# Kernel tuning notes

Measured on AMD Instinct MI355X. Metric: run time of the kernel, lower is better.

Reference implementation:

```python
import jax, jax.numpy as jnp
import numpy as np

N_NODES = 200000
D_FEAT = 128
B = 40000
DEG = 16
E = B * DEG
D_OUT = 256
N_CLASSES = 128


def setup_inputs() -> dict:
    key = jax.random.key(0)
    ks = jax.random.split(key, 8)
    inputs = jax.random.randint(ks[0], (B,), 0, N_NODES)
    neighbor_ids = jax.random.randint(ks[1], (E,), 0, N_NODES)
    segment_ids = jnp.repeat(jnp.arange(B, dtype=jnp.int64 if jax.config.jax_enable_x64 else jnp.int32), DEG)
    feat_data = jax.random.normal(ks[2], (N_NODES, D_FEAT), dtype=jnp.float32)
    W1 = jax.random.normal(ks[3], (D_OUT, 2 * D_FEAT), dtype=jnp.float32) * 0.05
    b1 = jax.random.normal(ks[4], (D_OUT,), dtype=jnp.float32) * 0.05
    W3 = jax.random.normal(ks[5], (N_CLASSES, D_OUT), dtype=jnp.float32) * 0.05
    b3 = jax.random.normal(ks[6], (N_CLASSES,), dtype=jnp.float32) * 0.05
    return {"inputs": inputs, "neighbor_ids": neighbor_ids, "segment_ids": segment_ids,
            "feat_data": feat_data, "W1": W1, "b1": b1, "W3": W3, "b3": b3}


def reference(inputs, neighbor_ids, segment_ids, feat_data, W1, b1, W3, b3):
    # Segment-mean over neighbor features (replaces Python per-node loop)
    neigh = feat_data[neighbor_ids]                               # [E, D]
    sums = jax.ops.segment_sum(neigh, segment_ids, num_segments=B)  # [B, D]
    cnt = jax.ops.segment_sum(jnp.ones((E,), jnp.float32), segment_ids, num_segments=B)
    means = sums / jnp.maximum(cnt, 1.0)[:, None]                 # [B, D]
    # Concat self + neighbor-mean, linear1
    emb = jnp.concatenate([feat_data[inputs], means], axis=1)     # [B, 2D]
    h = emb @ W1.T + b1                                           # [B, D_OUT]
    # ReLU -> linear3 -> L2 normalize (F.normalize, eps=1e-12)
    logits = jax.nn.relu(h) @ W3.T + b3                           # [B, n_classes]
    norm = jnp.linalg.norm(logits, axis=1, keepdims=True)
    return logits / jnp.maximum(norm, 1e-12)
```

## Files before the change

### kernel.cpp

```cpp
#include <hip/hip_runtime.h>
#include <stdint.h>

#define NNODES 200000
#define BNODES 40000
#define DEG    16
#define DFEAT  128
#define DOUT   256
#define NCLS   128
#define TILE   32

typedef __attribute__((ext_vector_type(8))) __bf16 bf16x8;
typedef __attribute__((ext_vector_type(4))) float  floatx4;

__device__ __forceinline__ uint32_t f2bf(float f) {
  uint32_t x = __float_as_uint(f);
  return ((x + 0x7fffu + ((x >> 16) & 1u)) >> 16) & 0xffffu;
}

__global__ void cvt_weights(const float* __restrict__ W1, const float* __restrict__ W3,
                            uint16_t* __restrict__ w1b, uint16_t* __restrict__ w3b) {
  int i = blockIdx.x * 256 + threadIdx.x;
  if (i < DOUT * 2 * DFEAT) w1b[i] = (uint16_t)f2bf(W1[i]);
  if (i < NCLS * DOUT)      w3b[i] = (uint16_t)f2bf(W3[i]);
}

__global__ __launch_bounds__(256) void sage_fused(
    const int* __restrict__ inputs, const int* __restrict__ nbr,
    const float* __restrict__ feat,
    const uint16_t* __restrict__ w1b, const float* __restrict__ b1,
    const uint16_t* __restrict__ w3b, const float* __restrict__ b3,
    float* __restrict__ out) {
  __shared__ __align__(16) uint16_t embL[TILE][264];
  __shared__ __align__(16) uint16_t hL[TILE][264];
  __shared__ __align__(16) float    lgL[TILE][132];

  const int tid  = threadIdx.x;
  const int w    = tid >> 6;
  const int lane = tid & 63;
  const int quad = lane >> 4;
  const int l16  = lane & 15;

  {
    const int nodeBase = blockIdx.x * TILE + w * 8;
#pragma unroll
    for (int n = 0; n < 8; ++n) {
      const int node = nodeBase + n;
      const int row  = w * 8 + n;
      const int* nb  = nbr + node * DEG;
      float sx = 0.f, sy = 0.f;
#pragma unroll
      for (int j = 0; j < DEG; ++j) {
        const float2 v = *(const float2*)(feat + (size_t)nb[j] * DFEAT + lane * 2);
        sx += v.x; sy += v.y;
      }
      const float2 sv = *(const float2*)(feat + (size_t)inputs[node] * DFEAT + lane * 2);
      const uint32_t selfp = f2bf(sv.x) | (f2bf(sv.y) << 16);
      const uint32_t meanp = f2bf(sx * 0.0625f) | (f2bf(sy * 0.0625f) << 16);
      *(uint32_t*)&embL[row][lane * 2]         = selfp;
      *(uint32_t*)&embL[row][DFEAT + lane * 2] = meanp;
    }
  }
  __syncthreads();

  const int kq = quad * 8;

  {
    floatx4 acc[2][4];
#pragma unroll
    for (int mt = 0; mt < 2; ++mt)
#pragma unroll
      for (int ot = 0; ot < 4; ++ot) {
        floatx4 z = {0.f, 0.f, 0.f, 0.f};
        acc[mt][ot] = z;
      }
#pragma unroll
    for (int kt = 0; kt < 8; ++kt) {
      const int k0 = kt * 32 + kq;
      const bf16x8 a0 = *(const bf16x8*)&embL[l16][k0];
      const bf16x8 a1 = *(const bf16x8*)&embL[16 + l16][k0];
#pragma unroll
      for (int ot = 0; ot < 4; ++ot) {
        const int o = (w * 4 + ot) * 16 + l16;
        const bf16x8 b = *(const bf16x8*)(w1b + o * 256 + k0);
        acc[0][ot] = __builtin_amdgcn_mfma_f32_16x16x32_bf16(a0, b, acc[0][ot], 0, 0, 0);
        acc[1][ot] = __builtin_amdgcn_mfma_f32_16x16x32_bf16(a1, b, acc[1][ot], 0, 0, 0);
      }
    }
#pragma unroll
    for (int ot = 0; ot < 4; ++ot) {
      const int o = (w * 4 + ot) * 16 + l16;
      const float bias = b1[o];
#pragma unroll
      for (int mt = 0; mt < 2; ++mt)
#pragma unroll
        for (int r = 0; r < 4; ++r) {
          float v = acc[mt][ot][r] + bias;
          v = fmaxf(v, 0.f);
          hL[mt * 16 + quad * 4 + r][o] = (uint16_t)f2bf(v);
        }
    }
  }
  __syncthreads();

  {
    floatx4 acc2[2][2];
#pragma unroll
    for (int mt = 0; mt < 2; ++mt)
#pragma unroll
      for (int ct = 0; ct < 2; ++ct) {
        floatx4 z = {0.f, 0.f, 0.f, 0.f};
        acc2[mt][ct] = z;
      }
#pragma unroll
    for (int kt = 0; kt < 8; ++kt) {
      const int k0 = kt * 32 + kq;
      const bf16x8 a0 = *(const bf16x8*)&hL[l16][k0];
      const bf16x8 a1 = *(const bf16x8*)&hL[16 + l16][k0];
#pragma unroll
      for (int ct = 0; ct < 2; ++ct) {
        const int c = (w * 2 + ct) * 16 + l16;
        const bf16x8 b = *(const bf16x8*)(w3b + c * 256 + k0);
        acc2[0][ct] = __builtin_amdgcn_mfma_f32_16x16x32_bf16(a0, b, acc2[0][ct], 0, 0, 0);
        acc2[1][ct] = __builtin_amdgcn_mfma_f32_16x16x32_bf16(a1, b, acc2[1][ct], 0, 0, 0);
      }
    }
#pragma unroll
    for (int ct = 0; ct < 2; ++ct) {
      const int c = (w * 2 + ct) * 16 + l16;
      const float bias = b3[c];
#pragma unroll
      for (int mt = 0; mt < 2; ++mt)
#pragma unroll
        for (int r = 0; r < 4; ++r)
          lgL[mt * 16 + quad * 4 + r][c] = acc2[mt][ct][r] + bias;
    }
  }
  __syncthreads();

  {
    const int nr  = tid >> 3;
    const int sub = tid & 7;
    const float* lrow = &lgL[nr][sub * 16];
    float4 v0 = *(const float4*)(lrow + 0);
    float4 v1 = *(const float4*)(lrow + 4);
    float4 v2 = *(const float4*)(lrow + 8);
    float4 v3 = *(const float4*)(lrow + 12);
    float ss = v0.x * v0.x + v0.y * v0.y + v0.z * v0.z + v0.w * v0.w
             + v1.x * v1.x + v1.y * v1.y + v1.z * v1.z + v1.w * v1.w
             + v2.x * v2.x + v2.y * v2.y + v2.z * v2.z + v2.w * v2.w
             + v3.x * v3.x + v3.y * v3.y + v3.z * v3.z + v3.w * v3.w;
    ss += __shfl_xor(ss, 1);
    ss += __shfl_xor(ss, 2);
    ss += __shfl_xor(ss, 4);
    const float scale = 1.f / fmaxf(sqrtf(ss), 1e-12f);
    v0.x *= scale; v0.y *= scale; v0.z *= scale; v0.w *= scale;
    v1.x *= scale; v1.y *= scale; v1.z *= scale; v1.w *= scale;
    v2.x *= scale; v2.y *= scale; v2.z *= scale; v2.w *= scale;
    v3.x *= scale; v3.y *= scale; v3.z *= scale; v3.w *= scale;
    float* op = out + ((size_t)(blockIdx.x * TILE + nr)) * NCLS + sub * 16;
    *(float4*)(op + 0)  = v0;
    *(float4*)(op + 4)  = v1;
    *(float4*)(op + 8)  = v2;
    *(float4*)(op + 12) = v3;
  }
}

extern "C" void kernel_launch(void* const* d_in, const int* in_sizes, int n_in,
                              void* d_out, int out_size, void* d_ws, size_t ws_size,
                              hipStream_t stream) {
  const int*   inputs = (const int*)d_in[0];
  const int*   nbr    = (const int*)d_in[1];
  const float* feat   = (const float*)d_in[3];
  const float* W1     = (const float*)d_in[4];
  const float* b1     = (const float*)d_in[5];
  const float* W3     = (const float*)d_in[6];
  const float* b3     = (const float*)d_in[7];

  uint16_t* w1b = (uint16_t*)d_ws;
  uint16_t* w3b = w1b + DOUT * 2 * DFEAT;

  cvt_weights<<<(DOUT * 2 * DFEAT) / 256, 256, 0, stream>>>(W1, W3, w1b, w3b);
  sage_fused<<<BNODES / TILE, 256, 0, stream>>>(inputs, nbr, feat, w1b, b1, w3b, b3,
                                                (float*)d_out);
}
```

Measured before the change: 218.0 us.

## Vectorize neighbor gather with float4 loads and overlap all row fetches

The gather stage now has each half-wave process one node, using 16-byte loads per lane. All 16 neighbor indices are fetched as int4 vectors and all 17 feature rows are loaded before summing, to raise memory-level parallelism on the random gather. The embedding and logits LDS buffers are aliased to cut shared memory, and launch bounds request 4 blocks per CU to raise occupancy. This costs more live registers per thread.

```diff
diff --git a/kernel.cpp b/kernel.cpp
--- a/kernel.cpp
+++ b/kernel.cpp
@@ -24,15 +24,16 @@
   if (i < NCLS * DOUT)      w3b[i] = (uint16_t)f2bf(W3[i]);
 }
 
-__global__ __launch_bounds__(256) void sage_fused(
+__global__ __launch_bounds__(256, 4) void sage_fused(
     const int* __restrict__ inputs, const int* __restrict__ nbr,
     const float* __restrict__ feat,
     const uint16_t* __restrict__ w1b, const float* __restrict__ b1,
     const uint16_t* __restrict__ w3b, const float* __restrict__ b3,
     float* __restrict__ out) {
-  __shared__ __align__(16) uint16_t embL[TILE][264];
+  __shared__ __align__(16) unsigned char smemA[TILE * 264 * 2];
   __shared__ __align__(16) uint16_t hL[TILE][264];
-  __shared__ __align__(16) float    lgL[TILE][132];
+  uint16_t (*embL)[264] = (uint16_t (*)[264])smemA;
+  float    (*lgL)[132]  = (float    (*)[132])smemA;
 
   const int tid  = threadIdx.x;
   const int w    = tid >> 6;
@@ -41,23 +42,38 @@
   const int l16  = lane & 15;
 
   {
+    const int h   = lane >> 5;
+    const int l32 = lane & 31;
+    const int col = l32 * 4;
     const int nodeBase = blockIdx.x * TILE + w * 8;
-#pragma unroll
-    for (int n = 0; n < 8; ++n) {
-      const int node = nodeBase + n;
-      const int row  = w * 8 + n;
+    const float* fb = feat + col;
+#pragma unroll
+    for (int p = 0; p < 4; ++p) {
+      const int node = nodeBase + p * 2 + h;
+      const int row  = w * 8 + p * 2 + h;
       const int* nb  = nbr + node * DEG;
-      float sx = 0.f, sy = 0.f;
-#pragma unroll
-      for (int j = 0; j < DEG; ++j) {
-        const float2 v = *(const float2*)(feat + (size_t)nb[j] * DFEAT + lane * 2);
-        sx += v.x; sy += v.y;
-      }
-      const float2 sv = *(const float2*)(feat + (size_t)inputs[node] * DFEAT + lane * 2);
-      const uint32_t selfp = f2bf(sv.x) | (f2bf(sv.y) << 16);
-      const uint32_t meanp = f2bf(sx * 0.0625f) | (f2bf(sy * 0.0625f) << 16);
-      *(uint32_t*)&embL[row][lane * 2]         = selfp;
-      *(uint32_t*)&embL[row][DFEAT + lane * 2] = meanp;
+      const int4 i0 = *(const int4*)(nb + 0);
+      const int4 i1 = *(const int4*)(nb + 4);
+      const int4 i2 = *(const int4*)(nb + 8);
+      const int4 i3 = *(const int4*)(nb + 12);
+      const int self = inputs[node];
+#define LDN(name, idx) const floatx4 name = *(const floatx4*)(fb + (size_t)(idx) * DFEAT)
+      LDN(v0,  i0.x); LDN(v1,  i0.y); LDN(v2,  i0.z); LDN(v3,  i0.w);
+      LDN(v4,  i1.x); LDN(v5,  i1.y); LDN(v6,  i1.z); LDN(v7,  i1.w);
+      LDN(v8,  i2.x); LDN(v9,  i2.y); LDN(v10, i2.z); LDN(v11, i2.w);
+      LDN(v12, i3.x); LDN(v13, i3.y); LDN(v14, i3.z); LDN(v15, i3.w);
+      LDN(sv, self);
+#undef LDN
+      const floatx4 s = (((v0 + v1) + (v2 + v3)) + ((v4 + v5) + (v6 + v7)))
+                      + (((v8 + v9) + (v10 + v11)) + ((v12 + v13) + (v14 + v15)));
+      const floatx4 m = s * 0.0625f;
+      uint2 selfp, meanp;
+      selfp.x = f2bf(sv.x) | (f2bf(sv.y) << 16);
+      selfp.y = f2bf(sv.z) | (f2bf(sv.w) << 16);
+      meanp.x = f2bf(m.x) | (f2bf(m.y) << 16);
+      meanp.y = f2bf(m.z) | (f2bf(m.w) << 16);
+      *(uint2*)&embL[row][col]         = selfp;
+      *(uint2*)&embL[row][DFEAT + col] = meanp;
     }
   }
   __syncthreads();
```

Measured after the change: 212.8 us. 2.3% less time.

## Widen neighbor gathers to 16-byte loads split across half-wavefronts, alias LDS buffers

Applied to the files above, without the earlier changes.

The gather phase now has each half-wavefront read a different neighbor row with float4 loads and combines the halves with a cross-lane shuffle. Two nodes are processed per iteration, so 16 independent loads are in flight per lane. The LDS buffers for the embedding tile and the logits tile now share storage, and launch bounds request 4 blocks per CU to raise occupancy. The cost is more registers per thread and extra shuffle work, which could limit how many waves fit on a CU.

```diff
diff --git a/kernel.cpp b/kernel.cpp
--- a/kernel.cpp
+++ b/kernel.cpp
@@ -17,47 +17,90 @@
   return ((x + 0x7fffu + ((x >> 16) & 1u)) >> 16) & 0xffffu;
 }
 
-__global__ void cvt_weights(const float* __restrict__ W1, const float* __restrict__ W3,
-                            uint16_t* __restrict__ w1b, uint16_t* __restrict__ w3b) {
+__global__ __launch_bounds__(256) void cvt_weights(
+    const float* __restrict__ W1, const float* __restrict__ W3,
+    uint16_t* __restrict__ w1b, uint16_t* __restrict__ w3b) {
   int i = blockIdx.x * 256 + threadIdx.x;
   if (i < DOUT * 2 * DFEAT) w1b[i] = (uint16_t)f2bf(W1[i]);
   if (i < NCLS * DOUT)      w3b[i] = (uint16_t)f2bf(W3[i]);
 }
 
-__global__ __launch_bounds__(256) void sage_fused(
+__global__ __launch_bounds__(256, 4) void sage_fused(
     const int* __restrict__ inputs, const int* __restrict__ nbr,
     const float* __restrict__ feat,
     const uint16_t* __restrict__ w1b, const float* __restrict__ b1,
     const uint16_t* __restrict__ w3b, const float* __restrict__ b3,
     float* __restrict__ out) {
-  __shared__ __align__(16) uint16_t embL[TILE][264];
+  __shared__ __align__(16) unsigned char smemA[TILE * 264 * 2];
   __shared__ __align__(16) uint16_t hL[TILE][264];
-  __shared__ __align__(16) float    lgL[TILE][132];
+  uint16_t (*embL)[264] = (uint16_t (*)[264])smemA;
+  float    (*lgL)[132]  = (float    (*)[132])smemA;
 
   const int tid  = threadIdx.x;
-  const int w    = tid >> 6;
+  const int w    = __builtin_amdgcn_readfirstlane(tid >> 6);
   const int lane = tid & 63;
   const int quad = lane >> 4;
   const int l16  = lane & 15;
 
   {
+    const int h   = lane >> 5;
+    const int l32 = lane & 31;
     const int nodeBase = blockIdx.x * TILE + w * 8;
-#pragma unroll
-    for (int n = 0; n < 8; ++n) {
-      const int node = nodeBase + n;
-      const int row  = w * 8 + n;
-      const int* nb  = nbr + node * DEG;
-      float sx = 0.f, sy = 0.f;
-#pragma unroll
-      for (int j = 0; j < DEG; ++j) {
-        const float2 v = *(const float2*)(feat + (size_t)nb[j] * DFEAT + lane * 2);
-        sx += v.x; sy += v.y;
-      }
-      const float2 sv = *(const float2*)(feat + (size_t)inputs[node] * DFEAT + lane * 2);
-      const uint32_t selfp = f2bf(sv.x) | (f2bf(sv.y) << 16);
-      const uint32_t meanp = f2bf(sx * 0.0625f) | (f2bf(sy * 0.0625f) << 16);
-      *(uint32_t*)&embL[row][lane * 2]         = selfp;
-      *(uint32_t*)&embL[row][DFEAT + lane * 2] = meanp;
+    const float* fcol = feat + l32 * 4;
+#pragma unroll
+    for (int pp = 0; pp < 8; pp += 2) {
+      const int nodeA = nodeBase + pp;
+      const int nodeB = nodeBase + pp + 1;
+      const int* nbA = nbr + nodeA * DEG;
+      const int* nbB = nbr + nodeB * DEG;
+      const int selfA = inputs[nodeA];
+      const int selfB = inputs[nodeB];
+      floatx4 a0, a1, a2, a3, a4, a5, a6, a7;
+      floatx4 c0, c1, c2, c3, c4, c5, c6, c7;
+#define LDP(dst, nb, g)                                                      \
+  {                                                                          \
+    const int id_ = h ? (nb)[2 * (g) + 1] : (nb)[2 * (g)];                   \
+    dst = *(const floatx4*)(fcol + (size_t)id_ * DFEAT);                     \
+  }
+      LDP(a0, nbA, 0) LDP(a1, nbA, 1) LDP(a2, nbA, 2) LDP(a3, nbA, 3)
+      LDP(a4, nbA, 4) LDP(a5, nbA, 5) LDP(a6, nbA, 6) LDP(a7, nbA, 7)
+      const float2 svA = *(const float2*)(feat + (size_t)selfA * DFEAT + lane * 2);
+      LDP(c0, nbB, 0) LDP(c1, nbB, 1) LDP(c2, nbB, 2) LDP(c3, nbB, 3)
+      LDP(c4, nbB, 4) LDP(c5, nbB, 5) LDP(c6, nbB, 6) LDP(c7, nbB, 7)
+      const float2 svB = *(const float2*)(feat + (size_t)selfB * DFEAT + lane * 2);
+#undef LDP
+      {
+        floatx4 s = ((a0 + a1) + (a2 + a3)) + ((a4 + a5) + (a6 + a7));
+        s.x += __shfl_xor(s.x, 32);
+        s.y += __shfl_xor(s.y, 32);
+        s.z += __shfl_xor(s.z, 32);
+        s.w += __shfl_xor(s.w, 32);
+        const floatx4 m = s * 0.0625f;
+        const int row = w * 8 + pp;
+        *(uint32_t*)&embL[row][lane * 2] = f2bf(svA.x) | (f2bf(svA.y) << 16);
+        if (h == 0) {
+          uint2 mp;
+          mp.x = f2bf(m.x) | (f2bf(m.y) << 16);
+          mp.y = f2bf(m.z) | (f2bf(m.w) << 16);
+          *(uint2*)&embL[row][DFEAT + l32 * 4] = mp;
+        }
+      }
+      {
+        floatx4 s = ((c0 + c1) + (c2 + c3)) + ((c4 + c5) + (c6 + c7));
+        s.x += __shfl_xor(s.x, 32);
+        s.y += __shfl_xor(s.y, 32);
+        s.z += __shfl_xor(s.z, 32);
+        s.w += __shfl_xor(s.w, 32);
+        const floatx4 m = s * 0.0625f;
+        const int row = w * 8 + pp + 1;
+        *(uint32_t*)&embL[row][lane * 2] = f2bf(svB.x) | (f2bf(svB.y) << 16);
+        if (h == 0) {
+          uint2 mp;
+          mp.x = f2bf(m.x) | (f2bf(m.y) << 16);
+          mp.y = f2bf(m.z) | (f2bf(m.w) << 16);
+          *(uint2*)&embL[row][DFEAT + l32 * 4] = mp;
+        }
+      }
     }
   }
   __syncthreads();
```

Result: no change. 218.9 us (+0.4%).

## Pre-convert feature table to bf16 and gather bf16 rows with smaller tiles

Applied to the files above, without the earlier changes.

Adds a kernel that converts the whole feature table to bf16 in workspace each call, so the neighbor gather reads half the bytes per row. The tile is halved to 16 nodes with more blocks and higher occupancy, gathers are batched per node pair for more memory-level parallelism, and the embedding buffer is aliased with the logits buffer in shared memory. The cost is a full extra read and write pass over the 100MB feature table per call, and neighbor sums are now taken over rounded values. If the workspace is too small it falls back to an fp32 path.

```diff
diff --git a/kernel.cpp b/kernel.cpp
--- a/kernel.cpp
+++ b/kernel.cpp
@@ -7,7 +7,7 @@
 #define DFEAT  128
 #define DOUT   256
 #define NCLS   128
-#define TILE   32
+#define TILE   16
 
 typedef __attribute__((ext_vector_type(8))) __bf16 bf16x8;
 typedef __attribute__((ext_vector_type(4))) float  floatx4;
@@ -16,48 +16,122 @@
   uint32_t x = __float_as_uint(f);
   return ((x + 0x7fffu + ((x >> 16) & 1u)) >> 16) & 0xffffu;
 }
-
-__global__ void cvt_weights(const float* __restrict__ W1, const float* __restrict__ W3,
-                            uint16_t* __restrict__ w1b, uint16_t* __restrict__ w3b) {
+__device__ __forceinline__ float bf2f(uint16_t u) {
+  return __uint_as_float((uint32_t)u << 16);
+}
+
+__global__ __launch_bounds__(256) void cvt_weights(
+    const float* __restrict__ W1, const float* __restrict__ W3,
+    uint16_t* __restrict__ w1b, uint16_t* __restrict__ w3b) {
   int i = blockIdx.x * 256 + threadIdx.x;
   if (i < DOUT * 2 * DFEAT) w1b[i] = (uint16_t)f2bf(W1[i]);
   if (i < NCLS * DOUT)      w3b[i] = (uint16_t)f2bf(W3[i]);
 }
 
-__global__ __launch_bounds__(256) void sage_fused(
+__global__ __launch_bounds__(256) void cvt_feat(
+    const float* __restrict__ feat, uint16_t* __restrict__ featb) {
+  const size_t i = ((size_t)blockIdx.x * 256 + threadIdx.x) * 16;
+  const float4 f0 = *(const float4*)(feat + i + 0);
+  const float4 f1 = *(const float4*)(feat + i + 4);
+  const float4 f2 = *(const float4*)(feat + i + 8);
+  const float4 f3 = *(const float4*)(feat + i + 12);
+  uint4 p0, p1;
+  p0.x = f2bf(f0.x) | (f2bf(f0.y) << 16);
+  p0.y = f2bf(f0.z) | (f2bf(f0.w) << 16);
+  p0.z = f2bf(f1.x) | (f2bf(f1.y) << 16);
+  p0.w = f2bf(f1.z) | (f2bf(f1.w) << 16);
+  p1.x = f2bf(f2.x) | (f2bf(f2.y) << 16);
+  p1.y = f2bf(f2.z) | (f2bf(f2.w) << 16);
+  p1.z = f2bf(f3.x) | (f2bf(f3.y) << 16);
+  p1.w = f2bf(f3.z) | (f2bf(f3.w) << 16);
+  *(uint4*)(featb + i)     = p0;
+  *(uint4*)(featb + i + 8) = p1;
+}
+
+template <bool BF16T>
+__global__ __launch_bounds__(256, 8) void sage_fused(
     const int* __restrict__ inputs, const int* __restrict__ nbr,
-    const float* __restrict__ feat,
+    const float* __restrict__ feat, const uint16_t* __restrict__ featb,
     const uint16_t* __restrict__ w1b, const float* __restrict__ b1,
     const uint16_t* __restrict__ w3b, const float* __restrict__ b3,
     float* __restrict__ out) {
-  __shared__ __align__(16) uint16_t embL[TILE][264];
+  __shared__ __align__(16) unsigned char smemA[TILE * 264 * 2];
   __shared__ __align__(16) uint16_t hL[TILE][264];
-  __shared__ __align__(16) float    lgL[TILE][132];
+  uint16_t (*embL)[264] = (uint16_t (*)[264])smemA;
+  float    (*lgL)[132]  = (float    (*)[132])smemA;
 
   const int tid  = threadIdx.x;
-  const int w    = tid >> 6;
+  const int w    = __builtin_amdgcn_readfirstlane(tid >> 6);
   const int lane = tid & 63;
   const int quad = lane >> 4;
   const int l16  = lane & 15;
 
   {
-    const int nodeBase = blockIdx.x * TILE + w * 8;
-#pragma unroll
-    for (int n = 0; n < 8; ++n) {
-      const int node = nodeBase + n;
-      const int row  = w * 8 + n;
-      const int* nb  = nbr + node * DEG;
-      float sx = 0.f, sy = 0.f;
-#pragma unroll
-      for (int j = 0; j < DEG; ++j) {
-        const float2 v = *(const float2*)(feat + (size_t)nb[j] * DFEAT + lane * 2);
-        sx += v.x; sy += v.y;
-      }
-      const float2 sv = *(const float2*)(feat + (size_t)inputs[node] * DFEAT + lane * 2);
-      const uint32_t selfp = f2bf(sv.x) | (f2bf(sv.y) << 16);
-      const uint32_t meanp = f2bf(sx * 0.0625f) | (f2bf(sy * 0.0625f) << 16);
-      *(uint32_t*)&embL[row][lane * 2]         = selfp;
-      *(uint32_t*)&embL[row][DFEAT + lane * 2] = meanp;
+    const int nodeBase = blockIdx.x * TILE + w * 4;
+    if constexpr (BF16T) {
+      const uint16_t* fb = featb + lane * 2;
+#pragma unroll
+      for (int p = 0; p < 4; p += 2) {
+        const int nA = nodeBase + p, nB = nodeBase + p + 1;
+        const int* nbA = nbr + nA * DEG;
+        const int* nbB = nbr + nB * DEG;
+        const int sA = inputs[nA], sB = inputs[nB];
+        ushort2 rA[16], rB[16];
+#pragma unroll
+        for (int j = 0; j < 16; ++j)
+          rA[j] = *(const ushort2*)(fb + (size_t)nbA[j] * DFEAT);
+        const ushort2 svA = *(const ushort2*)(fb + (size_t)sA * DFEAT);
+#pragma unroll
+        for (int j = 0; j < 16; ++j)
+          rB[j] = *(const ushort2*)(fb + (size_t)nbB[j] * DFEAT);
+        const ushort2 svB = *(const ushort2*)(fb + (size_t)sB * DFEAT);
+        {
+          const float sx = (((bf2f(rA[0].x) + bf2f(rA[1].x)) + (bf2f(rA[2].x) + bf2f(rA[3].x)))
+                          + ((bf2f(rA[4].x) + bf2f(rA[5].x)) + (bf2f(rA[6].x) + bf2f(rA[7].x))))
+                         + (((bf2f(rA[8].x) + bf2f(rA[9].x)) + (bf2f(rA[10].x) + bf2f(rA[11].x)))
+                          + ((bf2f(rA[12].x) + bf2f(rA[13].x)) + (bf2f(rA[14].x) + bf2f(rA[15].x))));
+          const float sy = (((bf2f(rA[0].y) + bf2f(rA[1].y)) + (bf2f(rA[2].y) + bf2f(rA[3].y)))
+                          + ((bf2f(rA[4].y) + bf2f(rA[5].y)) + (bf2f(rA[6].y) + bf2f(rA[7].y))))
+                         + (((bf2f(rA[8].y) + bf2f(rA[9].y)) + (bf2f(rA[10].y) + bf2f(rA[11].y)))
+                          + ((bf2f(rA[12].y) + bf2f(rA[13].y)) + (bf2f(rA[14].y) + bf2f(rA[15].y))));
+          const int row = w * 4 + p;
+          *(uint32_t*)&embL[row][lane * 2]         = (uint32_t)svA.x | ((uint32_t)svA.y << 16);
+          *(uint32_t*)&embL[row][DFEAT + lane * 2] = f2bf(sx * 0.0625f) | (f2bf(sy * 0.0625f) << 16);
+        }
+        {
+          const float sx = (((bf2f(rB[0].x) + bf2f(rB[1].x)) + (bf2f(rB[2].x) + bf2f(rB[3].x)))
+                          + ((bf2f(rB[4].x) + bf2f(rB[5].x)) + (bf2f(rB[6].x) + bf2f(rB[7].x))))
+                         + (((bf2f(rB[8].x) + bf2f(rB[9].x)) + (bf2f(rB[10].x) + bf2f(rB[11].x)))
+                          + ((bf2f(rB[12].x) + bf2f(rB[13].x)) + (bf2f(rB[14].x) + bf2f(rB[15].x))));
+          const float sy = (((bf2f(rB[0].y) + bf2f(rB[1].y)) + (bf2f(rB[2].y) + bf2f(rB[3].y)))
+                          + ((bf2f(rB[4].y) + bf2f(rB[5].y)) + (bf2f(rB[6].y) + bf2f(rB[7].y))))
+                         + (((bf2f(rB[8].y) + bf2f(rB[9].y)) + (bf2f(rB[10].y) + bf2f(rB[11].y)))
+                          + ((bf2f(rB[12].y) + bf2f(rB[13].y)) + (bf2f(rB[14].y) + bf2f(rB[15].y))));
+          const int row = w * 4 + p + 1;
+          *(uint32_t*)&embL[row][lane * 2]         = (uint32_t)svB.x | ((uint32_t)svB.y << 16);
+          *(uint32_t*)&embL[row][DFEAT + lane * 2] = f2bf(sx * 0.0625f) | (f2bf(sy * 0.0625f) << 16);
+        }
+      }
+    } else {
+      const float* fb = feat + lane * 2;
+#pragma unroll
+      for (int p = 0; p < 4; ++p) {
+        const int node = nodeBase + p;
+        const int* nb  = nbr + node * DEG;
+        const int self = inputs[node];
+        float2 r[16];
+#pragma unroll
+        for (int j = 0; j < 16; ++j)
+          r[j] = *(const float2*)(fb + (size_t)nb[j] * DFEAT);
+        const float2 sv = *(const float2*)(fb + (size_t)self * DFEAT);
+        const float sx = (((r[0].x + r[1].x) + (r[2].x + r[3].x)) + ((r[4].x + r[5].x) + (r[6].x + r[7].x)))
+                       + (((r[8].x + r[9].x) + (r[10].x + r[11].x)) + ((r[12].x + r[13].x) + (r[14].x + r[15].x)));
+        const float sy = (((r[0].y + r[1].y) + (r[2].y + r[3].y)) + ((r[4].y + r[5].y) + (r[6].y + r[7].y)))
+                       + (((r[8].y + r[9].y) + (r[10].y + r[11].y)) + ((r[12].y + r[13].y) + (r[14].y + r[15].y)));
+        const int row = w * 4 + p;
+        *(uint32_t*)&embL[row][lane * 2]         = f2bf(sv.x) | (f2bf(sv.y) << 16);
+        *(uint32_t*)&embL[row][DFEAT + lane * 2] = f2bf(sx * 0.0625f) | (f2bf(sy * 0.0625f) << 16);
+      }
     }
   }
   __syncthreads();
@@ -65,103 +139,84 @@
   const int kq = quad * 8;
 
   {
-    floatx4 acc[2][4];
-#pragma unroll
-    for (int mt = 0; mt < 2; ++mt)
-#pragma unroll
-      for (int ot = 0; ot < 4; ++ot) {
-        floatx4 z = {0.f, 0.f, 0.f, 0.f};
-        acc[mt][ot] = z;
-      }
+    floatx4 acc[4];
+#pragma unroll
+    for (int ot = 0; ot < 4; ++ot) {
+      floatx4 z = {0.f, 0.f, 0.f, 0.f};
+      acc[ot] = z;
+    }
 #pragma unroll
     for (int kt = 0; kt < 8; ++kt) {
       const int k0 = kt * 32 + kq;
-      const bf16x8 a0 = *(const bf16x8*)&embL[l16][k0];
-      const bf16x8 a1 = *(const bf16x8*)&embL[16 + l16][k0];
+      const bf16x8 a = *(const bf16x8*)&embL[l16][k0];
 #pragma unroll
       for (int ot = 0; ot < 4; ++ot) {
-        const int o = (w * 4 + ot) * 16 + l16;
+        const int o = w * 64 + ot * 16 + l16;
         const bf16x8 b = *(const bf16x8*)(w1b + o * 256 + k0);
-        acc[0][ot] = __builtin_amdgcn_mfma_f32_16x16x32_bf16(a0, b, acc[0][ot], 0, 0, 0);
-        acc[1][ot] = __builtin_amdgcn_mfma_f32_16x16x32_bf16(a1, b, acc[1][ot], 0, 0, 0);
+        acc[ot] = __builtin_amdgcn_mfma_f32_16x16x32_bf16(a, b, acc[ot], 0, 0, 0);
       }
     }
 #pragma unroll
     for (int ot = 0; ot < 4; ++ot) {
-      const int o = (w * 4 + ot) * 16 + l16;
+      const int o = w * 64 + ot * 16 + l16;
       const float bias = b1[o];
 #pragma unroll
-      for (int mt = 0; mt < 2; ++mt)
-#pragma unroll
-        for (int r = 0; r < 4; ++r) {
-          float v = acc[mt][ot][r] + bias;
-          v = fmaxf(v, 0.f);
-          hL[mt * 16 + quad * 4 + r][o] = (uint16_t)f2bf(v);
-        }
+      for (int r = 0; r < 4; ++r) {
+        float v = acc[ot][r] + bias;
+        v = fmaxf(v, 0.f);
+        hL[quad * 4 + r][o] = (uint16_t)f2bf(v);
+      }
     }
   }
   __syncthreads();
 
   {
-    floatx4 acc2[2][2];
-#pragma unroll
-    for (int mt = 0; mt < 2; ++mt)
-#pragma unroll
-      for (int ct = 0; ct < 2; ++ct) {
-        floatx4 z = {0.f, 0.f, 0.f, 0.f};
-        acc2[mt][ct] = z;
-      }
+    floatx4 acc2[2];
+#pragma unroll
+    for (int ct = 0; ct < 2; ++ct) {
+      floatx4 z = {0.f, 0.f, 0.f, 0.f};
+      acc2[ct] = z;
+    }
 #pragma unroll
     for (int kt = 0; kt < 8; ++kt) {
       const int k0 = kt * 32 + kq;
-      const bf16x8 a0 = *(const bf16x8*)&hL[l16][k0];
-      const bf16x8 a1 = *(const bf16x8*)&hL[16 + l16][k0];
+      const bf16x8 a = *(const bf16x8*)&hL[l16][k0];
 #pragma unroll
       for (int ct = 0; ct < 2; ++ct) {
-        const int c = (w * 2 + ct) * 16 + l16;
+        const int c = w * 32 + ct * 16 + l16;
         const bf16x8 b = *(const bf16x8*)(w3b + c * 256 + k0);
-        acc2[0][ct] = __builtin_amdgcn_mfma_f32_16x16x32_bf16(a0, b, acc2[0][ct], 0, 0, 0);
-        acc2[1][ct] = __builtin_amdgcn_mfma_f32_16x16x32_bf16(a1, b, acc2[1][ct], 0, 0, 0);
+        acc2[ct] = __builtin_amdgcn_mfma_f32_16x16x32_bf16(a, b, acc2[ct], 0, 0, 0);
       }
     }
 #pragma unroll
     for (int ct = 0; ct < 2; ++ct) {
-      const int c = (w * 2 + ct) * 16 + l16;
+      const int c = w * 32 + ct * 16 + l16;
       const float bias = b3[c];
 #pragma unroll
-      for (int mt = 0; mt < 2; ++mt)
-#pragma unroll
-        for (int r = 0; r < 4; ++r)
-          lgL[mt * 16 + quad * 4 + r][c] = acc2[mt][ct][r] + bias;
+      for (int r = 0; r < 4; ++r)
+        lgL[quad * 4 + r][c] = acc2[ct][r] + bias;
     }
   }
   __syncthreads();
 
   {
-    const int nr  = tid >> 3;
-    const int sub = tid & 7;
-    const float* lrow = &lgL[nr][sub * 16];
+    const int nr  = tid >> 4;
+    const int sub = tid & 15;
+    const float* lrow = &lgL[nr][sub * 8];
     float4 v0 = *(const float4*)(lrow + 0);
     float4 v1 = *(const float4*)(lrow + 4);
-    float4 v2 = *(const float4*)(lrow + 8);
-    float4 v3 = *(const float4*)(lrow + 12);
     float ss = v0.x * v0.x + v0.y * v0.y + v0.z * v0.z + v0.w * v0.w
-             + v1.x * v1.x + v1.y * v1.y + v1.z * v1.z + v1.w * v1.w
-             + v2.x * v2.x + v2.y * v2.y + v2.z * v2.z + v2.w * v2.w
-             + v3.x * v3.x + v3.y * v3.y + v3.z * v3.z + v3.w * v3.w;
+             + v1.x * v1.x + v1.y * v1.y + v1.z * v1.z + v1.w * v1.w;
     ss += __shfl_xor(ss, 1);
     ss += __shfl_xor(ss, 2);
     ss += __shfl_xor(ss, 4);
+    ss += __shfl_xor(ss, 8);
     const float scale = 1.f / fmaxf(sqrtf(ss), 1e-12f);
     v0.x *= scale; v0.y *= scale; v0.z *= scale; v0.w *= scale;
     v1.x *= scale; v1.y *= scale; v1.z *= scale; v1.w *= scale;
-    v2.x *= scale; v2.y *= scale; v2.z *= scale; v2.w *= scale;
-    v3.x *= scale; v3.y *= scale; v3.z *= scale; v3.w *= scale;
-    float* op = out + ((size_t)(blockIdx.x * TILE + nr)) * NCLS + sub * 16;
-    *(float4*)(op + 0)  = v0;
-    *(float4*)(op + 4)  = v1;
-    *(float4*)(op + 8)  = v2;
-    *(float4*)(op + 12) = v3;
+    float* op = out + ((size_t)(blockIdx.x * TILE + nr)) * NCLS + sub * 8;
+    *(float4*)(op + 0) = v0;
+    *(float4*)(op + 4) = v1;
   }
 }
 
@@ -176,10 +231,20 @@
   const float* W3     = (const float*)d_in[6];
   const float* b3     = (const float*)d_in[7];
 
-  uint16_t* w1b = (uint16_t*)d_ws;
-  uint16_t* w3b = w1b + DOUT * 2 * DFEAT;
+  uint16_t* w1b   = (uint16_t*)d_ws;
+  uint16_t* w3b   = w1b + DOUT * 2 * DFEAT;
+  uint16_t* featb = w3b + NCLS * DOUT;
+
+  const size_t need = ((size_t)(DOUT * 2 * DFEAT + NCLS * DOUT)
+                     + (size_t)NNODES * DFEAT) * sizeof(uint16_t);
 
   cvt_weights<<<(DOUT * 2 * DFEAT) / 256, 256, 0, stream>>>(W1, W3, w1b, w3b);
-  sage_fused<<<BNODES / TILE, 256, 0, stream>>>(inputs, nbr, feat, w1b, b1, w3b, b3,
-                                                (float*)d_out);
-}
+  if (ws_size >= need) {
+    cvt_feat<<<(NNODES * DFEAT) / (256 * 16), 256, 0, stream>>>(feat, featb);
+    sage_fused<true><<<BNODES / TILE, 256, 0, stream>>>(
+        inputs, nbr, feat, featb, w1b, b1, w3b, b3, (float*)d_out);
+  } else {
+    sage_fused<false><<<BNODES / TILE, 256, 0, stream>>>(
+        inputs, nbr, feat, nullptr, w1b, b1, w3b, b3, (float*)d_out);
+  }
+}
```

Measured after the change: 246.5 us. +13.1%, slower.
